# Optimization experiments

Measured on AMD Instinct MI355X. Metric: run time of the kernel, lower is better.

The kernel has to match this reference:

```python
import jax, jax.numpy as jnp
import numpy as np

D_MODEL = 1024
HEADS = 16
D_K = D_MODEL // HEADS
D_FF = 4096
B, S = 8, 1024
EPS = 1e-5
NEG = -1e9


def layer_norm(x, g, b):
    mu = jnp.mean(x, axis=-1, keepdims=True)
    var = jnp.var(x, axis=-1, keepdims=True)
    return (x - mu) * jax.lax.rsqrt(var + EPS) * g + b


def setup_inputs() -> dict:
    key = jax.random.key(0)
    ks = jax.random.split(key, 10)
    sc = lambda d: 1.0 / np.sqrt(d)
    return {
        "x": jax.random.normal(ks[0], (B, S, D_MODEL), jnp.float32),
        "mask": jnp.ones((B, 1, 1, S), jnp.int32),
        "wq": jax.random.normal(ks[1], (D_MODEL, D_MODEL), jnp.float32) * sc(D_MODEL),
        "bq": jnp.zeros((D_MODEL,), jnp.float32),
        "wk": jax.random.normal(ks[2], (D_MODEL, D_MODEL), jnp.float32) * sc(D_MODEL),
        "bk": jnp.zeros((D_MODEL,), jnp.float32),
        "wv": jax.random.normal(ks[3], (D_MODEL, D_MODEL), jnp.float32) * sc(D_MODEL),
        "bv": jnp.zeros((D_MODEL,), jnp.float32),
        "wo": jax.random.normal(ks[4], (D_MODEL, D_MODEL), jnp.float32) * sc(D_MODEL),
        "bo": jnp.zeros((D_MODEL,), jnp.float32),
        "w1": jax.random.normal(ks[5], (D_MODEL, D_FF), jnp.float32) * sc(D_MODEL),
        "b1": jnp.zeros((D_FF,), jnp.float32),
        "w2": jax.random.normal(ks[6], (D_FF, D_MODEL), jnp.float32) * sc(D_FF),
        "b2": jnp.zeros((D_MODEL,), jnp.float32),
        "ln1_g": jnp.ones((D_MODEL,), jnp.float32),
        "ln1_b": jnp.zeros((D_MODEL,), jnp.float32),
        "ln2_g": jnp.ones((D_MODEL,), jnp.float32),
        "ln2_b": jnp.zeros((D_MODEL,), jnp.float32),
    }


def reference(x, mask, wq, bq, wk, bk, wv, bv, wo, bo, w1, b1, w2, b2,
              ln1_g, ln1_b, ln2_g, ln2_b):
    b, s, d = x.shape

    # --- self-attention sublayer with residual + LN (pre-norm, dropout=0) ---
    h = layer_norm(x, ln1_g, ln1_b)
    q = (h @ wq + bq).reshape(b, s, HEADS, D_K).transpose(0, 2, 1, 3)  # [b,h,s,dk]
    k = (h @ wk + bk).reshape(b, s, HEADS, D_K).transpose(0, 2, 1, 3)
    v = (h @ wv + bv).reshape(b, s, HEADS, D_K).transpose(0, 2, 1, 3)

    scores = jnp.einsum("bhqd,bhkd->bhqk", q, k) / np.sqrt(D_K)  # [b,h,s,s]
    scores = jnp.where(mask == 0, NEG, scores)
    attn = jax.nn.softmax(scores, axis=-1)
    ctx = jnp.einsum("bhqk,bhkd->bhqd", attn, v)
    ctx = ctx.transpose(0, 2, 1, 3).reshape(b, s, d)
    x = x + (ctx @ wo + bo)

    # --- feed-forward sublayer with residual + LN ---
    h2 = layer_norm(x, ln2_g, ln2_b)
    ff = jax.nn.relu(h2 @ w1 + b1) @ w2 + b2
    return x + ff
```

## Files before the change

kernel.cpp:

```cpp
#include <hip/hip_runtime.h>
#include <hip/hip_bf16.h>

typedef __attribute__((ext_vector_type(8))) __bf16 bf16x8;
typedef __attribute__((ext_vector_type(4))) __bf16 bf16x4;
typedef __attribute__((ext_vector_type(4))) float  f32x4;

__device__ __forceinline__ void gload_lds16(const __bf16* g, __bf16* l) {
    __builtin_amdgcn_global_load_lds(
        (const __attribute__((address_space(1))) void*)g,
        (__attribute__((address_space(3))) void*)l, 16, 0, 0);
}

#define SOFT_BARRIER()                                            \
    do {                                                          \
        asm volatile("s_waitcnt lgkmcnt(0)" ::: "memory");        \
        __builtin_amdgcn_s_barrier();                             \
        asm volatile("" ::: "memory");                            \
    } while (0)

__global__ __launch_bounds__(256) void transpose_all(
    const float* __restrict__ wq, const float* __restrict__ wk,
    const float* __restrict__ wv, const float* __restrict__ wo,
    const float* __restrict__ w1, const float* __restrict__ w2,
    __bf16* __restrict__ wqkvT, __bf16* __restrict__ woT,
    __bf16* __restrict__ w1T, __bf16* __restrict__ w2T,
    const float* __restrict__ bq, const float* __restrict__ bk,
    const float* __restrict__ bv, float* __restrict__ bqkv) {
    __shared__ float t[32][33];
    const int bid = blockIdx.x;
    if (bid >= 12288) {
        const int i = (bid - 12288) * 256 + threadIdx.x;
        bqkv[i] = bq[i]; bqkv[1024 + i] = bk[i]; bqkv[2048 + i] = bv[i];
        return;
    }
    const float* in; __bf16* out; int K, N, nb, kb;
    if (bid < 4096) {
        const int which = bid >> 10, tt = bid & 1023;
        K = 1024; N = 1024;
        in  = which == 0 ? wq : which == 1 ? wk : which == 2 ? wv : wo;
        out = which == 3 ? woT : wqkvT + (size_t)which * 1048576;
        nb = (tt & 31) * 32; kb = (tt >> 5) * 32;
    } else if (bid < 8192) {
        const int tt = bid - 4096;
        in = w1; out = w1T; K = 1024; N = 4096;
        nb = (tt & 127) * 32; kb = (tt >> 7) * 32;
    } else {
        const int tt = bid - 8192;
        in = w2; out = w2T; K = 4096; N = 1024;
        nb = (tt & 31) * 32; kb = (tt >> 5) * 32;
    }
    const int tx = threadIdx.x & 31, ty = threadIdx.x >> 5;
#pragma unroll
    for (int i = 0; i < 32; i += 8)
        t[ty + i][tx] = in[(size_t)(kb + ty + i) * N + nb + tx];
    __syncthreads();
#pragma unroll
    for (int i = 0; i < 32; i += 8)
        out[(size_t)(nb + ty + i) * K + kb + tx] = (__bf16)t[tx][ty + i];
}

__global__ __launch_bounds__(256) void ln_to_bf16(const float* __restrict__ x,
                                                  const float* __restrict__ g,
                                                  const float* __restrict__ bb,
                                                  __bf16* __restrict__ out) {
    const int row = blockIdx.x, t = threadIdx.x;
    const float4 v = ((const float4*)(x + (size_t)row * 1024))[t];
    float s  = v.x + v.y + v.z + v.w;
    float ss = v.x * v.x + v.y * v.y + v.z * v.z + v.w * v.w;
#pragma unroll
    for (int off = 32; off; off >>= 1) {
        s  += __shfl_down(s, off);
        ss += __shfl_down(ss, off);
    }
    __shared__ float ps[4], pss[4];
    if ((t & 63) == 0) { ps[t >> 6] = s; pss[t >> 6] = ss; }
    __syncthreads();
    s  = ps[0] + ps[1] + ps[2] + ps[3];
    ss = pss[0] + pss[1] + pss[2] + pss[3];
    const float mu   = s * (1.0f / 1024.0f);
    const float var  = ss * (1.0f / 1024.0f) - mu * mu;
    const float rinv = rsqrtf(var + 1e-5f);
    const float4 gv = ((const float4*)g)[t];
    const float4 bv = ((const float4*)bb)[t];
    bf16x4 o;
    o[0] = (__bf16)((v.x - mu) * rinv * gv.x + bv.x);
    o[1] = (__bf16)((v.y - mu) * rinv * gv.y + bv.y);
    o[2] = (__bf16)((v.z - mu) * rinv * gv.z + bv.z);
    o[3] = (__bf16)((v.w - mu) * rinv * gv.w + bv.w);
    *(bf16x4*)(out + (size_t)row * 1024 + 4 * t) = o;
}

template <int MODE>
__global__ __launch_bounds__(512, 2) void gemm256(const __bf16* __restrict__ A,
                                                  const __bf16* __restrict__ BT,
                                                  const float* __restrict__ bias,
                                                  __bf16* __restrict__ outp,
                                                  int M, int N, int K, int NMB) {
    __shared__ __align__(16) __bf16 lds[65536];
    const int bid = blockIdx.x;
    const int c8 = bid & 7, loc = bid >> 3;
    const int MH = NMB >> 3;
    const int bm = (c8 * MH + loc % MH) * 256;
    const int bn = (loc / MH) * 256;
    const int tid = threadIdx.x, l = tid & 63, w = tid >> 6;
    const int wm = (w >> 2) * 128, wn = (w & 3) * 64;
    const int lg = l >> 4, lm = l & 15;
    const int NT = K >> 6;

    const __bf16* gsrc[4];
    int ldst[4];
#pragma unroll
    for (int j = 0; j < 4; ++j) {
        const unsigned X = (unsigned)(((j & 1) << 13) + (w << 10) + l * 16);
        const unsigned L = X ^ (((X >> 7) & 7u) << 4);
        const int row = L >> 6, col = (L & 63) >> 1;
        gsrc[j] = (j < 2 ? A + (size_t)(bm + row) * K : BT + (size_t)(bn + row) * K) + col;
        ldst[j] = ((j < 2 ? 0 : 16384) + ((j & 1) << 13) + (w << 10)) >> 1;
    }
    int aoff[2][4], boff[4];
#pragma unroll
    for (int mh = 0; mh < 2; ++mh)
#pragma unroll
        for (int fr = 0; fr < 4; ++fr) {
            const unsigned Lb = (unsigned)(wm + mh * 64 + fr * 16 + lm) * 64 + lg * 16;
            aoff[mh][fr] = (int)(Lb ^ (((Lb >> 7) & 7u) << 4)) >> 1;
        }
#pragma unroll
    for (int n = 0; n < 4; ++n) {
        const unsigned Lb = (unsigned)(wn + n * 16 + lm) * 64 + lg * 16;
        boff[n] = (int)(16384u + (Lb ^ (((Lb >> 7) & 7u) << 4))) >> 1;
    }

    f32x4 acc[8][4];
#pragma unroll
    for (int m = 0; m < 8; ++m)
#pragma unroll
        for (int n = 0; n < 4; ++n) acc[m][n] = f32x4{0.f, 0.f, 0.f, 0.f};

#define ISSUE_SUB(u)                                                          \
    do {                                                                      \
        __bf16* sbp = lds + (((u) & 3) << 14);                                \
        const int go = (u) << 5;                                              \
        _Pragma("unroll")                                                     \
        for (int j = 0; j < 4; ++j) gload_lds16(gsrc[j] + go, sbp + ldst[j]); \
    } while (0)

#define MFMA16(MH_, BREG)                                                     \
    do {                                                                      \
        __builtin_amdgcn_s_setprio(1);                                        \
        _Pragma("unroll")                                                     \
        for (int i = 0; i < 4; ++i)                                           \
            _Pragma("unroll")                                                 \
            for (int n = 0; n < 4; ++n)                                       \
                acc[(MH_)*4 + i][n] = __builtin_amdgcn_mfma_f32_16x16x32_bf16(\
                    af[i], BREG[n], acc[(MH_)*4 + i][n], 0, 0, 0);            \
        __builtin_amdgcn_s_setprio(0);                                        \
    } while (0)

    ISSUE_SUB(0); ISSUE_SUB(1); ISSUE_SUB(2); ISSUE_SUB(3);
    asm volatile("s_waitcnt vmcnt(8)" ::: "memory");
    __builtin_amdgcn_s_barrier();

    for (int t = 0; t < NT; ++t) {
        const int sa = ((2 * t) & 3) << 14, sb = ((2 * t + 1) & 3) << 14;
        bf16x8 af[4], b0[4], b1[4];
#pragma unroll
        for (int fr = 0; fr < 4; ++fr) af[fr] = *(const bf16x8*)(lds + sa + aoff[0][fr]);
#pragma unroll
        for (int n = 0; n < 4; ++n) b0[n] = *(const bf16x8*)(lds + sa + boff[n]);
        asm volatile("" ::: "memory");
        __builtin_amdgcn_s_barrier();
        __builtin_amdgcn_sched_barrier(0);
        MFMA16(0, b0);
        __builtin_amdgcn_sched_barrier(0);
        __builtin_amdgcn_s_barrier();
#pragma unroll
        for (int fr = 0; fr < 4; ++fr) af[fr] = *(const bf16x8*)(lds + sa + aoff[1][fr]);
        asm volatile("" ::: "memory");
        __builtin_amdgcn_s_barrier();
        __builtin_amdgcn_sched_barrier(0);
        MFMA16(1, b0);
        __builtin_amdgcn_sched_barrier(0);
        __builtin_amdgcn_s_barrier();
        if (t < NT - 2) ISSUE_SUB(2 * t + 4);
#pragma unroll
        for (int fr = 0; fr < 4; ++fr) af[fr] = *(const bf16x8*)(lds + sb + aoff[0][fr]);
#pragma unroll
        for (int n = 0; n < 4; ++n) b1[n] = *(const bf16x8*)(lds + sb + boff[n]);
        asm volatile("" ::: "memory");
        __builtin_amdgcn_s_barrier();
        __builtin_amdgcn_sched_barrier(0);
        MFMA16(0, b1);
        __builtin_amdgcn_sched_barrier(0);
        __builtin_amdgcn_s_barrier();
#pragma unroll
        for (int fr = 0; fr < 4; ++fr) af[fr] = *(const bf16x8*)(lds + sb + aoff[1][fr]);
        asm volatile("" ::: "memory");
        __builtin_amdgcn_s_barrier();
        __builtin_amdgcn_sched_barrier(0);
        MFMA16(1, b1);
        __builtin_amdgcn_sched_barrier(0);
        __builtin_amdgcn_s_barrier();
        if (t < NT - 2) {
            ISSUE_SUB(2 * t + 5);
            asm volatile("s_waitcnt vmcnt(8)" ::: "memory");
        } else if (t == NT - 2) {
            asm volatile("s_waitcnt vmcnt(0)" ::: "memory");
        }
        __builtin_amdgcn_s_barrier();
    }
#undef ISSUE_SUB
#undef MFMA16

#pragma unroll
    for (int m = 0; m < 8; ++m) {
        const int row = bm + wm + (m >> 2) * 64 + (m & 3) * 16 + lg * 4;
#pragma unroll
        for (int n = 0; n < 4; ++n) {
            const int col = bn + wn + n * 16 + lm;
            const float bvv = bias[col];
#pragma unroll
            for (int r = 0; r < 4; ++r) {
                const float v = acc[m][n][r] + bvv;
                outp[(size_t)(row + r) * N + col] =
                    (MODE == 1) ? (__bf16)fmaxf(v, 0.f) : (__bf16)v;
            }
        }
    }
}

__global__ __launch_bounds__(512, 4) void gemm128x128(const __bf16* __restrict__ A,
                                                      const __bf16* __restrict__ BT,
                                                      const float* __restrict__ bias,
                                                      const float* __restrict__ resid,
                                                      float* __restrict__ outp,
                                                      int M, int N, int K, int NMB) {
    __shared__ __align__(16) __bf16 lds[32768];
    const int bid = blockIdx.x;
    const int c8 = bid & 7, loc = bid >> 3;
    const int MH = NMB >> 3;
    const int bm = (c8 * MH + loc % MH) * 128;
    const int bn = (loc / MH) * 128;
    const int tid = threadIdx.x, l = tid & 63, w = tid >> 6;
    const int wm = (w >> 1) * 32, wn = (w & 1) * 64;
    const int lg = l >> 4, lm = l & 15;
    const int NT = K >> 6;

    const __bf16* gsrc[2];
    int ldst[2];
#pragma unroll
    for (int j = 0; j < 2; ++j) {
        const unsigned X = (unsigned)(tid * 16);
        const unsigned L = X ^ (((X >> 7) & 7u) << 4);
        const int row = L >> 6, col = (L & 63) >> 1;
        gsrc[j] = (j == 0 ? A + (size_t)(bm + row) * K : BT + (size_t)(bn + row) * K) + col;
        ldst[j] = ((j == 0 ? 0 : 8192) + (w << 10)) >> 1;
    }
    int aoff[2], boff[4];
#pragma unroll
    for (int mh = 0; mh < 2; ++mh) {
        const unsigned Lb = (unsigned)(wm + mh * 16 + lm) * 64 + lg * 16;
        aoff[mh] = (int)(Lb ^ (((Lb >> 7) & 7u) << 4)) >> 1;
    }
#pragma unroll
    for (int n = 0; n < 4; ++n) {
        const unsigned Lb = (unsigned)(wn + n * 16 + lm) * 64 + lg * 16;
        boff[n] = (int)(8192u + (Lb ^ (((Lb >> 7) & 7u) << 4))) >> 1;
    }

    f32x4 acc[2][4];
#pragma unroll
    for (int m = 0; m < 2; ++m)
#pragma unroll
        for (int n = 0; n < 4; ++n) acc[m][n] = f32x4{0.f, 0.f, 0.f, 0.f};

#define ISSUE_SUB(u)                                                          \
    do {                                                                      \
        __bf16* sbp = lds + (((u) & 3) << 13);                                \
        const int go = (u) << 5;                                              \
        _Pragma("unroll")                                                     \
        for (int j = 0; j < 2; ++j) gload_lds16(gsrc[j] + go, sbp + ldst[j]); \
    } while (0)

#define PHASE8(SBASE)                                                         \
    do {                                                                      \
        bf16x8 a0 = *(const bf16x8*)(lds + (SBASE) + aoff[0]);                \
        bf16x8 a1 = *(const bf16x8*)(lds + (SBASE) + aoff[1]);                \
        bf16x8 bfr[4];                                                        \
        _Pragma("unroll")                                                     \
        for (int n = 0; n < 4; ++n)                                           \
            bfr[n] = *(const bf16x8*)(lds + (SBASE) + boff[n]);               \
        asm volatile("" ::: "memory");                                        \
        __builtin_amdgcn_s_barrier();                                         \
        __builtin_amdgcn_sched_barrier(0);                                    \
        __builtin_amdgcn_s_setprio(1);                                        \
        _Pragma("unroll")                                                     \
        for (int n = 0; n < 4; ++n)                                           \
            acc[0][n] = __builtin_amdgcn_mfma_f32_16x16x32_bf16(              \
                a0, bfr[n], acc[0][n], 0, 0, 0);                              \
        _Pragma("unroll")                                                     \
        for (int n = 0; n < 4; ++n)                                           \
            acc[1][n] = __builtin_amdgcn_mfma_f32_16x16x32_bf16(              \
                a1, bfr[n], acc[1][n], 0, 0, 0);                              \
        __builtin_amdgcn_s_setprio(0);                                        \
        __builtin_amdgcn_sched_barrier(0);                                    \
        __builtin_amdgcn_s_barrier();                                         \
    } while (0)

    ISSUE_SUB(0); ISSUE_SUB(1); ISSUE_SUB(2); ISSUE_SUB(3);
    asm volatile("s_waitcnt vmcnt(4)" ::: "memory");
    __builtin_amdgcn_s_barrier();

    for (int t = 0; t < NT; ++t) {
        const int sa = ((2 * t) & 3) << 13, sb = ((2 * t + 1) & 3) << 13;
        PHASE8(sa);
        if (t < NT - 2) ISSUE_SUB(2 * t + 4);
        PHASE8(sb);
        if (t < NT - 2) {
            ISSUE_SUB(2 * t + 5);
            asm volatile("s_waitcnt vmcnt(4)" ::: "memory");
        } else if (t == NT - 2) {
            asm volatile("s_waitcnt vmcnt(0)" ::: "memory");
        }
        __builtin_amdgcn_s_barrier();
    }
#undef ISSUE_SUB
#undef PHASE8

#pragma unroll
    for (int m = 0; m < 2; ++m) {
        const int row = bm + wm + m * 16 + lg * 4;
#pragma unroll
        for (int n = 0; n < 4; ++n) {
            const int col = bn + wn + n * 16 + lm;
            const float bvv = bias[col];
#pragma unroll
            for (int r = 0; r < 4; ++r) {
                const size_t idx = (size_t)(row + r) * N + col;
                outp[idx] = resid[idx] + acc[m][n][r] + bvv;
            }
        }
    }
}

__global__ __launch_bounds__(512, 2) void gemm_qkv(const __bf16* __restrict__ A,
                                                   const __bf16* __restrict__ BT,
                                                   const float* __restrict__ bias,
                                                   __bf16* __restrict__ outp,
                                                   __bf16* __restrict__ vTout,
                                                   int M, int N, int K, int NMB) {
    __shared__ __align__(16) __bf16 lds[49152];
    const int bid = blockIdx.x;
    const int c8 = bid & 7, loc = bid >> 3;
    const int MH = NMB >> 3;
    const int bm = (c8 * MH + loc % MH) * 128;
    const int bn = (loc / MH) * 256;
    const int tid = threadIdx.x, l = tid & 63, w = tid >> 6;
    const int wm = (w >> 2) * 64, wn = (w & 3) * 64;
    const int lg = l >> 4, lm = l & 15;
    const int NT = K >> 6;

    const __bf16* gsrc[3];
    int ldst[3];
#pragma unroll
    for (int j = 0; j < 3; ++j) {
        const unsigned X = (unsigned)((j == 0 ? 0 : (j - 1) * 8192) + tid * 16);
        const unsigned L = X ^ (((X >> 7) & 7u) << 4);
        const int row = L >> 6, col = (L & 63) >> 1;
        gsrc[j] = (j == 0 ? A + (size_t)(bm + row) * K : BT + (size_t)(bn + row) * K) + col;
        ldst[j] = ((j == 0 ? 0 : 8192 + (j - 1) * 8192) + (w << 10)) >> 1;
    }
    int aoff[2][2], boff[4];
#pragma unroll
    for (int mh = 0; mh < 2; ++mh)
#pragma unroll
        for (int fr = 0; fr < 2; ++fr) {
            const unsigned Lb = (unsigned)(wm + mh * 32 + fr * 16 + lm) * 64 + lg * 16;
            aoff[mh][fr] = (int)(Lb ^ (((Lb >> 7) & 7u) << 4)) >> 1;
        }
#pragma unroll
    for (int n = 0; n < 4; ++n) {
        const unsigned Lb = (unsigned)(wn + n * 16 + lm) * 64 + lg * 16;
        boff[n] = (int)(8192u + (Lb ^ (((Lb >> 7) & 7u) << 4))) >> 1;
    }

    f32x4 acc[4][4];
#pragma unroll
    for (int m = 0; m < 4; ++m)
#pragma unroll
        for (int n = 0; n < 4; ++n) acc[m][n] = f32x4{0.f, 0.f, 0.f, 0.f};

#define ISSUE_SUB(u)                                                          \
    do {                                                                      \
        __bf16* sbp = lds + ((u) & 3) * 12288;                                \
        const int go = (u) << 5;                                              \
        _Pragma("unroll")                                                     \
        for (int j = 0; j < 3; ++j) gload_lds16(gsrc[j] + go, sbp + ldst[j]); \
    } while (0)

#define PHASE16(SBASE)                                                        \
    do {                                                                      \
        bf16x8 afr[2][2], bfr[4];                                             \
        _Pragma("unroll")                                                     \
        for (int mh = 0; mh < 2; ++mh)                                        \
            _Pragma("unroll")                                                 \
            for (int fr = 0; fr < 2; ++fr)                                    \
                afr[mh][fr] = *(const bf16x8*)(lds + (SBASE) + aoff[mh][fr]); \
        _Pragma("unroll")                                                     \
        for (int n = 0; n < 4; ++n)                                           \
            bfr[n] = *(const bf16x8*)(lds + (SBASE) + boff[n]);               \
        asm volatile("" ::: "memory");                                        \
        __builtin_amdgcn_s_barrier();                                         \
        __builtin_amdgcn_sched_barrier(0);                                    \
        __builtin_amdgcn_s_setprio(1);                                        \
        _Pragma("unroll")                                                     \
        for (int mh = 0; mh < 2; ++mh)                                        \
            _Pragma("unroll")                                                 \
            for (int fr = 0; fr < 2; ++fr)                                    \
                _Pragma("unroll")                                             \
                for (int n = 0; n < 4; ++n)                                   \
                    acc[mh * 2 + fr][n] =                                     \
                        __builtin_amdgcn_mfma_f32_16x16x32_bf16(              \
                            afr[mh][fr], bfr[n], acc[mh * 2 + fr][n], 0, 0, 0);\
        __builtin_amdgcn_s_setprio(0);                                        \
        __builtin_amdgcn_sched_barrier(0);                                    \
        __builtin_amdgcn_s_barrier();                                         \
    } while (0)

    ISSUE_SUB(0); ISSUE_SUB(1); ISSUE_SUB(2); ISSUE_SUB(3);
    asm volatile("s_waitcnt vmcnt(6)" ::: "memory");
    __builtin_amdgcn_s_barrier();

    for (int t = 0; t < NT; ++t) {
        const int sa = ((2 * t) & 3) * 12288, sb = ((2 * t + 1) & 3) * 12288;
        PHASE16(sa);
        if (t < NT - 2) ISSUE_SUB(2 * t + 4);
        PHASE16(sb);
        if (t < NT - 2) {
            ISSUE_SUB(2 * t + 5);
            asm volatile("s_waitcnt vmcnt(6)" ::: "memory");
        } else if (t == NT - 2) {
            asm volatile("s_waitcnt vmcnt(0)" ::: "memory");
        }
        __builtin_amdgcn_s_barrier();
    }
#undef ISSUE_SUB
#undef PHASE16

    const bool isQ = bn < 1024;
#pragma unroll
    for (int m = 0; m < 4; ++m) {
        const int row = bm + wm + m * 16 + lg * 4;
#pragma unroll
        for (int n = 0; n < 4; ++n) {
            const int col = bn + wn + n * 16 + lm;
            const float bvv = bias[col];
            if (bn >= 2048) {
                bf16x4 o;
#pragma unroll
                for (int r = 0; r < 4; ++r) o[r] = (__bf16)(acc[m][n][r] + bvv);
                const int s = row & 1023;
                const int sp = (s & ~31) | (((s >> 2) & 3) << 3) | (((s >> 4) & 1) << 2);
                *(bf16x4*)(vTout + (size_t)((row >> 10) * 1024 + (col - 2048)) * 1024 +
                           sp) = o;
            } else {
#pragma unroll
                for (int r = 0; r < 4; ++r) {
                    float v = acc[m][n][r] + bvv;
                    if (isQ) v *= 0.18033688f;
                    outp[(size_t)(row + r) * 2048 + col] = (__bf16)v;
                }
            }
        }
    }
}

__global__ __launch_bounds__(512, 4) void attn_kernel(const __bf16* __restrict__ qk,
                                                      const __bf16* __restrict__ vT,
                                                      const int* __restrict__ mask,
                                                      __bf16* __restrict__ ctx) {
    const int h = blockIdx.x, qt = blockIdx.y, b = blockIdx.z;
    const int tid = threadIdx.x, w = tid >> 6, l = tid & 63;
    const int lg = l >> 4, lm = l & 15;

    __shared__ __align__(16) __bf16 Ks[2][64][76];
    __shared__ __align__(16) __bf16 Vt[2][64][76];

    const int qrow = qt * 128 + w * 16 + lm;
    const __bf16* qp = qk + (size_t)(b * 1024 + qrow) * 2048 + h * 64 + lg * 8;
    bf16x8 aq[2];
    aq[0] = *(const bf16x8*)qp;
    aq[1] = *(const bf16x8*)(qp + 32);

    const int r0 = tid >> 3, cc0 = (tid & 7) * 8;
    const __bf16* kbase = qk + (size_t)(b * 1024 + r0) * 2048 + 1024 + h * 64 + cc0;
    const __bf16* vbase = vT + (size_t)(b * 1024 + h * 64 + r0) * 1024 + cc0;
    uint4 kreg, vreg;
#define ALOAD(kt)                                                      \
    do {                                                               \
        kreg = *(const uint4*)(kbase + (size_t)(kt) * 64 * 2048);      \
        vreg = *(const uint4*)(vbase + (kt) * 64);                     \
    } while (0)
#define AWRITE(bf)                                                     \
    do {                                                               \
        *(uint4*)&Ks[bf][r0][cc0] = kreg;                              \
        *(uint4*)&Vt[bf][r0][cc0] = vreg;                              \
    } while (0)

    ALOAD(0); AWRITE(0); ALOAD(1);
    SOFT_BARRIER();

    const int* mbase = mask + b * 1024;
    float mrun = -1e30f, lsum = 0.f;
    f32x4 oacc[4];
#pragma unroll
    for (int n = 0; n < 4; ++n) oacc[n] = f32x4{0.f, 0.f, 0.f, 0.f};

    for (int kt = 0; kt < 16; ++kt) {
        const int cur = kt & 1;
        if (kt < 15) AWRITE(cur ^ 1);
        if (kt < 14) ALOAD(kt + 2);
        f32x4 sacc[4];
        int4 mk4[4];
#pragma unroll
        for (int n = 0; n < 4; ++n) {
            mk4[n] = *(const int4*)(mbase + kt * 64 + n * 16 + lg * 4);
            sacc[n] = f32x4{0.f, 0.f, 0.f, 0.f};
#pragma unroll
            for (int kk = 0; kk < 2; ++kk) {
                bf16x8 bk = *(const bf16x8*)&Ks[cur][n * 16 + lm][lg * 8 + kk * 32];
                sacc[n] = __builtin_amdgcn_mfma_f32_16x16x32_bf16(bk, aq[kk], sacc[n], 0, 0, 0);
            }
        }
        float p[4][4], mn[4];
#pragma unroll
        for (int n = 0; n < 4; ++n) {
            p[n][0] = mk4[n].x ? sacc[n][0] : -1e9f;
            p[n][1] = mk4[n].y ? sacc[n][1] : -1e9f;
            p[n][2] = mk4[n].z ? sacc[n][2] : -1e9f;
            p[n][3] = mk4[n].w ? sacc[n][3] : -1e9f;
            mn[n] = fmaxf(fmaxf(p[n][0], p[n][1]), fmaxf(p[n][2], p[n][3]));
        }
        float mloc = fmaxf(fmaxf(mn[0], mn[1]), fmaxf(mn[2], mn[3]));
        mloc = fmaxf(mloc, __shfl_xor(mloc, 16));
        mloc = fmaxf(mloc, __shfl_xor(mloc, 32));
        const float pm = fmaxf(mrun, mloc);
        if (!__all(pm - mrun <= 11.5f)) {
            const float sc = exp2f(mrun - pm);
            mrun = pm;
            lsum *= sc;
#pragma unroll
            for (int n = 0; n < 4; ++n)
#pragma unroll
                for (int r = 0; r < 4; ++r) oacc[n][r] *= sc;
        }
        float rsn[4];
#pragma unroll
        for (int n = 0; n < 4; ++n) {
#pragma unroll
            for (int r = 0; r < 4; ++r) p[n][r] = exp2f(p[n][r] - mrun);
            rsn[n] = (p[n][0] + p[n][1]) + (p[n][2] + p[n][3]);
        }
        float rs = (rsn[0] + rsn[1]) + (rsn[2] + rsn[3]);
        rs += __shfl_xor(rs, 16);
        rs += __shfl_xor(rs, 32);
        lsum += rs;
#pragma unroll
        for (int kk = 0; kk < 2; ++kk) {
            bf16x8 pfrag;
#pragma unroll
            for (int r = 0; r < 4; ++r) {
                pfrag[r]     = (__bf16)p[2 * kk][r];
                pfrag[4 + r] = (__bf16)p[2 * kk + 1][r];
            }
#pragma unroll
            for (int nd = 0; nd < 4; ++nd) {
                bf16x8 vf = *(const bf16x8*)&Vt[cur][nd * 16 + lm][lg * 8 + kk * 32];
                oacc[nd] = __builtin_amdgcn_mfma_f32_16x16x32_bf16(vf, pfrag, oacc[nd], 0, 0, 0);
            }
        }
        SOFT_BARRIER();
    }
#undef ALOAD
#undef AWRITE
    const float rinv = 1.0f / lsum;
#pragma unroll
    for (int nd = 0; nd < 4; ++nd) {
        bf16x4 o;
#pragma unroll
        for (int r = 0; r < 4; ++r) o[r] = (__bf16)(oacc[nd][r] * rinv);
        *(bf16x4*)(ctx + (size_t)(b * 1024 + qrow) * 1024 + h * 64 + nd * 16 + lg * 4) = o;
    }
}

extern "C" void kernel_launch(void* const* d_in, const int* in_sizes, int n_in,
                              void* d_out, int out_size, void* d_ws, size_t ws_size,
                              hipStream_t stream) {
    const float* x    = (const float*)d_in[0];
    const int*   mask = (const int*)d_in[1];
    const float* wq   = (const float*)d_in[2];
    const float* bq   = (const float*)d_in[3];
    const float* wk   = (const float*)d_in[4];
    const float* bk   = (const float*)d_in[5];
    const float* wv   = (const float*)d_in[6];
    const float* bv   = (const float*)d_in[7];
    const float* wo   = (const float*)d_in[8];
    const float* bo   = (const float*)d_in[9];
    const float* w1   = (const float*)d_in[10];
    const float* b1   = (const float*)d_in[11];
    const float* w2   = (const float*)d_in[12];
    const float* b2   = (const float*)d_in[13];
    const float* ln1g = (const float*)d_in[14];
    const float* ln1b = (const float*)d_in[15];
    const float* ln2g = (const float*)d_in[16];
    const float* ln2b = (const float*)d_in[17];
    float* out = (float*)d_out;
    char* ws = (char*)d_ws;

    __bf16* wqkvT = (__bf16*)(ws + 0);
    __bf16* woT   = (__bf16*)(ws + 6291456);
    __bf16* w1T   = (__bf16*)(ws + 8388608);
    __bf16* w2T   = (__bf16*)(ws + 16777216);
    float*  bqkv  = (float*)(ws + 25165824);
    __bf16* hb    = (__bf16*)(ws + 25178112);
    __bf16* qkb   = (__bf16*)(ws + 41955328);
    __bf16* vTb   = (__bf16*)(ws + 75509760);
    __bf16* ctxb  = (__bf16*)(ws + 92286976);
    __bf16* ff1b  = qkb;

    transpose_all<<<12292, 256, 0, stream>>>(wq, wk, wv, wo, w1, w2,
                                             wqkvT, woT, w1T, w2T,
                                             bq, bk, bv, bqkv);

    ln_to_bf16<<<8192, 256, 0, stream>>>(x, ln1g, ln1b, hb);
    gemm_qkv<<<768, 512, 0, stream>>>(hb, wqkvT, bqkv, qkb, vTb, 8192, 3072, 1024, 64);
    attn_kernel<<<dim3(16, 8, 8), 512, 0, stream>>>(qkb, vTb, mask, ctxb);
    gemm128x128<<<512, 512, 0, stream>>>(ctxb, woT, bo, x, out, 8192, 1024, 1024, 64);
    ln_to_bf16<<<8192, 256, 0, stream>>>(out, ln2g, ln2b, hb);
    gemm256<1><<<512, 512, 0, stream>>>(hb, w1T, b1, ff1b, 8192, 4096, 1024, 32);
    gemm128x128<<<512, 512, 0, stream>>>(ff1b, w2T, b2, out, out, 8192, 1024, 4096, 64);
}
```

Before: 369.8 us.

## Enlarge output-projection and FFN2 GEMM tiles to 256x128

```diff
diff --git a/kernel.cpp b/kernel.cpp
--- a/kernel.cpp
+++ b/kernel.cpp
@@ -229,77 +229,76 @@
     }
 }
 
-__global__ __launch_bounds__(512, 4) void gemm128x128(const __bf16* __restrict__ A,
+__global__ __launch_bounds__(512, 2) void gemm256x128(const __bf16* __restrict__ A,
                                                       const __bf16* __restrict__ BT,
                                                       const float* __restrict__ bias,
                                                       const float* __restrict__ resid,
                                                       float* __restrict__ outp,
                                                       int M, int N, int K, int NMB) {
-    __shared__ __align__(16) __bf16 lds[32768];
+    __shared__ __align__(16) __bf16 lds[49152];
     const int bid = blockIdx.x;
     const int c8 = bid & 7, loc = bid >> 3;
     const int MH = NMB >> 3;
-    const int bm = (c8 * MH + loc % MH) * 128;
+    const int bm = (c8 * MH + loc % MH) * 256;
     const int bn = (loc / MH) * 128;
     const int tid = threadIdx.x, l = tid & 63, w = tid >> 6;
-    const int wm = (w >> 1) * 32, wn = (w & 1) * 64;
     const int lg = l >> 4, lm = l & 15;
     const int NT = K >> 6;
 
-    const __bf16* gsrc[2];
-    int ldst[2];
-#pragma unroll
-    for (int j = 0; j < 2; ++j) {
-        const unsigned X = (unsigned)(tid * 16);
+    const __bf16* gsrc[3];
+    int ldst[3];
+#pragma unroll
+    for (int j = 0; j < 3; ++j) {
+        const unsigned X = (unsigned)((j == 1 ? 8192 : 0) + tid * 16);
         const unsigned L = X ^ (((X >> 7) & 7u) << 4);
         const int row = L >> 6, col = (L & 63) >> 1;
-        gsrc[j] = (j == 0 ? A + (size_t)(bm + row) * K : BT + (size_t)(bn + row) * K) + col;
-        ldst[j] = ((j == 0 ? 0 : 8192) + (w << 10)) >> 1;
-    }
-    int aoff[2], boff[4];
-#pragma unroll
-    for (int mh = 0; mh < 2; ++mh) {
-        const unsigned Lb = (unsigned)(wm + mh * 16 + lm) * 64 + lg * 16;
-        aoff[mh] = (int)(Lb ^ (((Lb >> 7) & 7u) << 4)) >> 1;
-    }
-#pragma unroll
-    for (int n = 0; n < 4; ++n) {
-        const unsigned Lb = (unsigned)(wn + n * 16 + lm) * 64 + lg * 16;
-        boff[n] = (int)(8192u + (Lb ^ (((Lb >> 7) & 7u) << 4))) >> 1;
-    }
-
-    f32x4 acc[2][4];
+        gsrc[j] = (j < 2 ? A + (size_t)(bm + row) * K : BT + (size_t)(bn + row) * K) + col;
+        ldst[j] = ((j < 2 ? (j << 13) : 16384) + (w << 10)) >> 1;
+    }
+    int aoff[2], boff[8];
+#pragma unroll
+    for (int fr = 0; fr < 2; ++fr) {
+        const unsigned Lb = (unsigned)(w * 32 + fr * 16 + lm) * 64 + lg * 16;
+        aoff[fr] = (int)(Lb ^ (((Lb >> 7) & 7u) << 4)) >> 1;
+    }
+#pragma unroll
+    for (int n = 0; n < 8; ++n) {
+        const unsigned Lb = (unsigned)(n * 16 + lm) * 64 + lg * 16;
+        boff[n] = (int)(16384u + (Lb ^ (((Lb >> 7) & 7u) << 4))) >> 1;
+    }
+
+    f32x4 acc[2][8];
 #pragma unroll
     for (int m = 0; m < 2; ++m)
 #pragma unroll
-        for (int n = 0; n < 4; ++n) acc[m][n] = f32x4{0.f, 0.f, 0.f, 0.f};
+        for (int n = 0; n < 8; ++n) acc[m][n] = f32x4{0.f, 0.f, 0.f, 0.f};
 
 #define ISSUE_SUB(u)                                                          \
     do {                                                                      \
-        __bf16* sbp = lds + (((u) & 3) << 13);                                \
+        __bf16* sbp = lds + ((u) & 3) * 12288;                                \
         const int go = (u) << 5;                                              \
         _Pragma("unroll")                                                     \
-        for (int j = 0; j < 2; ++j) gload_lds16(gsrc[j] + go, sbp + ldst[j]); \
-    } while (0)
-
-#define PHASE8(SBASE)                                                         \
+        for (int j = 0; j < 3; ++j) gload_lds16(gsrc[j] + go, sbp + ldst[j]); \
+    } while (0)
+
+#define PHASEFAT(SBASE)                                                       \
     do {                                                                      \
         bf16x8 a0 = *(const bf16x8*)(lds + (SBASE) + aoff[0]);                \
         bf16x8 a1 = *(const bf16x8*)(lds + (SBASE) + aoff[1]);                \
-        bf16x8 bfr[4];                                                        \
-        _Pragma("unroll")                                                     \
-        for (int n = 0; n < 4; ++n)                                           \
+        bf16x8 bfr[8];                                                        \
+        _Pragma("unroll")                                                     \
+        for (int n = 0; n < 8; ++n)                                           \
             bfr[n] = *(const bf16x8*)(lds + (SBASE) + boff[n]);               \
         asm volatile("" ::: "memory");                                        \
         __builtin_amdgcn_s_barrier();                                         \
         __builtin_amdgcn_sched_barrier(0);                                    \
         __builtin_amdgcn_s_setprio(1);                                        \
         _Pragma("unroll")                                                     \
-        for (int n = 0; n < 4; ++n)                                           \
+        for (int n = 0; n < 8; ++n)                                           \
             acc[0][n] = __builtin_amdgcn_mfma_f32_16x16x32_bf16(              \
                 a0, bfr[n], acc[0][n], 0, 0, 0);                              \
         _Pragma("unroll")                                                     \
-        for (int n = 0; n < 4; ++n)                                           \
+        for (int n = 0; n < 8; ++n)                                           \
             acc[1][n] = __builtin_amdgcn_mfma_f32_16x16x32_bf16(              \
                 a1, bfr[n], acc[1][n], 0, 0, 0);                              \
         __builtin_amdgcn_s_setprio(0);                                        \
@@ -308,31 +307,31 @@
     } while (0)
 
     ISSUE_SUB(0); ISSUE_SUB(1); ISSUE_SUB(2); ISSUE_SUB(3);
-    asm volatile("s_waitcnt vmcnt(4)" ::: "memory");
+    asm volatile("s_waitcnt vmcnt(6)" ::: "memory");
     __builtin_amdgcn_s_barrier();
 
     for (int t = 0; t < NT; ++t) {
-        const int sa = ((2 * t) & 3) << 13, sb = ((2 * t + 1) & 3) << 13;
-        PHASE8(sa);
+        const int sa = ((2 * t) & 3) * 12288, sb = ((2 * t + 1) & 3) * 12288;
+        PHASEFAT(sa);
         if (t < NT - 2) ISSUE_SUB(2 * t + 4);
-        PHASE8(sb);
+        PHASEFAT(sb);
         if (t < NT - 2) {
             ISSUE_SUB(2 * t + 5);
-            asm volatile("s_waitcnt vmcnt(4)" ::: "memory");
+            asm volatile("s_waitcnt vmcnt(6)" ::: "memory");
         } else if (t == NT - 2) {
             asm volatile("s_waitcnt vmcnt(0)" ::: "memory");
         }
         __builtin_amdgcn_s_barrier();
     }
 #undef ISSUE_SUB
-#undef PHASE8
+#undef PHASEFAT
 
 #pragma unroll
     for (int m = 0; m < 2; ++m) {
-        const int row = bm + wm + m * 16 + lg * 4;
-#pragma unroll
-        for (int n = 0; n < 4; ++n) {
-            const int col = bn + wn + n * 16 + lm;
+        const int row = bm + w * 32 + m * 16 + lg * 4;
+#pragma unroll
+        for (int n = 0; n < 8; ++n) {
+            const int col = bn + n * 16 + lm;
             const float bvv = bias[col];
 #pragma unroll
             for (int r = 0; r < 4; ++r) {
@@ -498,7 +497,7 @@
     uint4 kreg, vreg;
 #define ALOAD(kt)                                                      \
     do {                                                               \
-        kreg = *(const uint4*)(kbase + (size_t)(kt) * 64 * 2048);      \
+        kreg = *(const uint4*)(kbase + (size_t)(kt) * 131072);         \
         vreg = *(const uint4*)(vbase + (kt) * 64);                     \
     } while (0)
 #define AWRITE(bf)                                                     \
@@ -635,8 +634,8 @@
     ln_to_bf16<<<8192, 256, 0, stream>>>(x, ln1g, ln1b, hb);
     gemm_qkv<<<768, 512, 0, stream>>>(hb, wqkvT, bqkv, qkb, vTb, 8192, 3072, 1024, 64);
     attn_kernel<<<dim3(16, 8, 8), 512, 0, stream>>>(qkb, vTb, mask, ctxb);
-    gemm128x128<<<512, 512, 0, stream>>>(ctxb, woT, bo, x, out, 8192, 1024, 1024, 64);
+    gemm256x128<<<256, 512, 0, stream>>>(ctxb, woT, bo, x, out, 8192, 1024, 1024, 32);
     ln_to_bf16<<<8192, 256, 0, stream>>>(out, ln2g, ln2b, hb);
     gemm256<1><<<512, 512, 0, stream>>>(hb, w1T, b1, ff1b, 8192, 4096, 1024, 32);
-    gemm128x128<<<512, 512, 0, stream>>>(ff1b, w2T, b2, out, out, 8192, 1024, 4096, 64);
-}
+    gemm256x128<<<256, 512, 0, stream>>>(ff1b, w2T, b2, out, out, 8192, 1024, 4096, 32);
+}
```

New measurement: 366.8 us. Within noise of the previous version (-0.8%).
